# Optimization experiments

Hardware: AMD Instinct MI355X
Metric: run time of the kernel (lower is better)

## Reference

```python
import jax, jax.numpy as jnp
import numpy as np

DIM = 1024
HEADS = 16
DH = 64          # dim_for_head
INNER = HEADS * DH
SCALE = DH ** -0.5


def setup_inputs() -> dict:
    key = jax.random.key(0)
    ks = jax.random.split(key, 5)
    x = jax.random.normal(ks[0], (4, 2048, DIM), dtype=jnp.float32)
    ln_gamma = jnp.ones((DIM,), dtype=jnp.float32)
    ln_beta = jnp.zeros((DIM,), dtype=jnp.float32)
    # torch Linear weight is [out, in]; store same layout, apply as x @ W.T
    w_qkv = jax.random.normal(ks[1], (3 * INNER, DIM), dtype=jnp.float32) * (DIM ** -0.5)
    w_out = jax.random.normal(ks[2], (DIM, INNER), dtype=jnp.float32) * (INNER ** -0.5)
    b_out = jnp.zeros((DIM,), dtype=jnp.float32)
    return {"x": x, "ln_gamma": ln_gamma, "ln_beta": ln_beta,
            "w_qkv": w_qkv, "w_out": w_out, "b_out": b_out}


def reference(x, ln_gamma, ln_beta, w_qkv, w_out, b_out):
    b, n, d = x.shape
    # LayerNorm (eps=1e-5 as torch default)
    mu = jnp.mean(x, axis=-1, keepdims=True)
    var = jnp.mean(jnp.square(x - mu), axis=-1, keepdims=True)
    xn = (x - mu) * jax.lax.rsqrt(var + 1e-5) * ln_gamma + ln_beta
    # QKV projection
    qkv = xn @ w_qkv.T                                   # [b, n, 3*inner]
    q, k, v = jnp.split(qkv, 3, axis=-1)
    reshape = lambda t: t.reshape(b, n, HEADS, DH).transpose(0, 2, 1, 3)  # [b, h, n, d]
    q, k, v = reshape(q), reshape(k), reshape(v)
    # Attention
    dots = jnp.einsum('bhqd,bhkd->bhqk', q, k) * SCALE
    attn = jax.nn.softmax(dots, axis=-1)                 # dropout p=0 -> identity
    out = jnp.einsum('bhqk,bhkd->bhqd', attn, v)
    out = out.transpose(0, 2, 1, 3).reshape(b, n, INNER)
    return out @ w_out.T + b_out
```

## Files before the change

### kernel.cpp

```cpp
#include <hip/hip_runtime.h>
#include <stdint.h>


typedef __attribute__((ext_vector_type(4)))  float  f32x4;
typedef __attribute__((ext_vector_type(16))) float  f32x16;
typedef __attribute__((ext_vector_type(8)))  short  s16x8;
typedef __attribute__((ext_vector_type(4)))  unsigned short u16x4;
typedef __attribute__((ext_vector_type(2)))  int    i32x2;
typedef __attribute__((ext_vector_type(4)))  int    i32x4;

__device__ __forceinline__ float bf2f(short b) {
    union { unsigned u; float f; } x; x.u = ((unsigned)(unsigned short)b) << 16; return x.f;
}
__device__ __forceinline__ short f2bf(float f) {
    union { float f; unsigned u; } x; x.f = f;
    unsigned r = x.u + 0x7fffu + ((x.u >> 16) & 1u);
    return (short)(r >> 16);
}
__device__ __forceinline__ float exp2_hw(float x) {
    float r; asm("v_exp_f32 %0, %1" : "=v"(r) : "v"(x)); return r;
}

__device__ __forceinline__ void gload_lds16(const void* g, void* l) {
    __builtin_amdgcn_global_load_lds(
        (const __attribute__((address_space(1))) void*)g,
        (__attribute__((address_space(3))) void*)l, 16, 0, 0);
}

__global__ void cvt_bf16(const float* __restrict__ in, short* __restrict__ out, int n4) {
    int i = blockIdx.x * blockDim.x + threadIdx.x;
    if (i >= n4) return;
    f32x4 v = ((const f32x4*)in)[i];
    u16x4 o;
    o.x = (unsigned short)f2bf(v.x); o.y = (unsigned short)f2bf(v.y);
    o.z = (unsigned short)f2bf(v.z); o.w = (unsigned short)f2bf(v.w);
    ((u16x4*)out)[i] = o;
}

__global__ void cvt_wqkv(const float* __restrict__ in, short* __restrict__ out, int n4) {
    int i = blockIdx.x * blockDim.x + threadIdx.x;
    if (i >= n4) return;
    const int row = i >> 8;
    const float sc = (row < 1024) ? 0.18033688011112042f : 1.0f;
    f32x4 v = ((const f32x4*)in)[i];
    u16x4 o;
    o.x = (unsigned short)f2bf(v.x * sc); o.y = (unsigned short)f2bf(v.y * sc);
    o.z = (unsigned short)f2bf(v.z * sc); o.w = (unsigned short)f2bf(v.w * sc);
    ((u16x4*)out)[i] = o;
}

__global__ __launch_bounds__(256)
void ln_kernel(const float* __restrict__ x, const float* __restrict__ gamma,
               const float* __restrict__ beta, short* __restrict__ xn) {
    const int w = threadIdx.x >> 6, l = threadIdx.x & 63;
    const size_t row = (size_t)blockIdx.x * 4 + w;
    const float* xr = x + row * 1024;
    f32x4 v[4];
    float sum = 0.f, ss = 0.f;
#pragma unroll
    for (int i = 0; i < 4; i++) {
        v[i] = *(const f32x4*)(xr + (l + 64 * i) * 4);
#pragma unroll
        for (int e = 0; e < 4; e++) { sum += v[i][e]; ss += v[i][e] * v[i][e]; }
    }
#pragma unroll
    for (int d = 1; d < 64; d <<= 1) { sum += __shfl_xor(sum, d); ss += __shfl_xor(ss, d); }
    const float mu   = sum * (1.f / 1024.f);
    const float var  = ss * (1.f / 1024.f) - mu * mu;
    const float rstd = rsqrtf(var + 1e-5f);
#pragma unroll
    for (int i = 0; i < 4; i++) {
        f32x4 g  = *(const f32x4*)(gamma + (l + 64 * i) * 4);
        f32x4 bt = *(const f32x4*)(beta  + (l + 64 * i) * 4);
        u16x4 o;
#pragma unroll
        for (int e = 0; e < 4; e++)
            o[e] = (unsigned short)f2bf((v[i][e] - mu) * rstd * g[e] + bt[e]);
        *(u16x4*)(xn + row * 1024 + (l + 64 * i) * 4) = o;
    }
}

template <int NX>
__global__ __launch_bounds__(512, 2)
void gemm256(const short* __restrict__ A, const short* __restrict__ W,
             short* __restrict__ outb, int M, int N, int K) {
    extern __shared__ short smem[];
    short* Albuf = smem;
    short* Blbuf = smem + 32768;
    const int tid = threadIdx.x;
    const int w = tid >> 6, l = tid & 63;
    const int wr = w >> 2, wc = w & 3;
    const int nb = gridDim.x, bid = blockIdx.x;
    const int swz = (bid & 7) * (nb >> 3) + (bid >> 3);
    const int m0 = (swz / NX) * 256, n0 = (swz % NX) * 192;
    const int lx = l & 15, hi4 = l >> 4, l7 = l & 7;
    const int srow = l >> 3;
    const int scs  = (l & 7) ^ srow;

    f32x4 acc[8][3];
#pragma unroll
    for (int i = 0; i < 8; i++)
#pragma unroll
        for (int j = 0; j < 3; j++) acc[i][j] = (f32x4)0.f;

    auto STAGE = [&](int buf, int t) {
        const int k0 = t * 64;
#pragma unroll
        for (int p = 0; p < 4; p++) {
            const int row = p * 64 + w * 8 + srow;
            gload_lds16(A + (size_t)(m0 + row) * K + k0 + scs * 8,
                        Albuf + buf * 16384 + (p * 64 + w * 8) * 64);
        }
#pragma unroll
        for (int p = 0; p < 3; p++) {
            const int row = p * 64 + w * 8 + srow;
            gload_lds16(W + (size_t)(n0 + row) * K + k0 + scs * 8,
                        Blbuf + buf * 12288 + (p * 64 + w * 8) * 64);
        }
    };

    STAGE(0, 0);
    const int NT = K >> 6;
    for (int t = 0; t < NT; ++t) {
        const int cur = t & 1;
        if (t + 1 < NT) {
            STAGE(cur ^ 1, t + 1);
            asm volatile("s_waitcnt vmcnt(7)" ::: "memory");
        } else {
            asm volatile("s_waitcnt vmcnt(0)" ::: "memory");
        }
        __builtin_amdgcn_s_barrier();
        const short* Ab = Albuf + cur * 16384;
        const short* Bb = Blbuf + cur * 12288;

        s16x8 bfr[2][3];
#pragma unroll
        for (int kc = 0; kc < 2; kc++)
#pragma unroll
            for (int j = 0; j < 3; j++) {
                const int R = wc * 48 + j * 16 + lx;
                bfr[kc][j] = *(const s16x8*)(Bb + R * 64 + (((kc * 4 + hi4) ^ l7) * 8));
            }

#pragma unroll
        for (int p = 0; p < 4; p++) {
            s16x8 afr[2][2];
#pragma unroll
            for (int ii = 0; ii < 2; ii++)
#pragma unroll
                for (int kc = 0; kc < 2; kc++) {
                    const int R = wr * 128 + (p * 2 + ii) * 16 + lx;
                    afr[ii][kc] = *(const s16x8*)(Ab + R * 64 + (((kc * 4 + hi4) ^ l7) * 8));
                }
            __builtin_amdgcn_s_barrier();
            __builtin_amdgcn_s_setprio(1);
#pragma unroll
            for (int kc = 0; kc < 2; kc++)
#pragma unroll
                for (int ii = 0; ii < 2; ii++)
#pragma unroll
                    for (int j = 0; j < 3; j++)
                        acc[p * 2 + ii][j] = __builtin_amdgcn_mfma_f32_16x16x32_bf16(
                            afr[ii][kc], bfr[kc][j], acc[p * 2 + ii][j], 0, 0, 0);
            __builtin_amdgcn_s_setprio(0);
            __builtin_amdgcn_s_barrier();
        }
    }

    const int lr = hi4 * 4;
#pragma unroll
    for (int i = 0; i < 8; i++) {
        const int rb = m0 + wr * 128 + i * 16 + lr;
#pragma unroll
        for (int j = 0; j < 3; j++) {
            const int cc = n0 + wc * 48 + j * 16 + lx;
#pragma unroll
            for (int r = 0; r < 4; r++)
                outb[(size_t)(rb + r) * N + cc] = f2bf(acc[i][j][r]);
        }
    }
}

template <int MODE, int NX>
__global__ __launch_bounds__(256)
void gemm_bt(const short* __restrict__ A, const short* __restrict__ W,
             short* __restrict__ outb, float* __restrict__ outf,
             const float* __restrict__ bias, int M, int N, int K) {
    __shared__ short Al[128 * 64];
    __shared__ short Bl[128 * 64];
    const int tid = threadIdx.x;
    const int w = tid >> 6, l = tid & 63;
    const int wr = w >> 1, wc = w & 1;
    const int nb = gridDim.x, bid = blockIdx.x;
    const int swz = (bid & 7) * (nb >> 3) + (bid >> 3);
    const int m0 = (swz / NX) * 128, n0 = (swz % NX) * 128;
    const int r8 = tid >> 3;
    const int c8 = tid & 7;

    f32x4 acc[4][4];
#pragma unroll
    for (int i = 0; i < 4; i++)
#pragma unroll
        for (int j = 0; j < 4; j++) acc[i][j] = (f32x4)0.f;

    for (int k0 = 0; k0 < K; k0 += 64) {
        __syncthreads();
#pragma unroll
        for (int p = 0; p < 4; p++) {
            const int row = p * 32 + r8;
            gload_lds16(A + (size_t)(m0 + row) * K + k0 + c8 * 8, Al + (p * 32 + w * 8) * 64);
            gload_lds16(W + (size_t)(n0 + row) * K + k0 + c8 * 8, Bl + (p * 32 + w * 8) * 64);
        }
        __syncthreads();
#pragma unroll
        for (int kc = 0; kc < 2; kc++) {
            const int ko = kc * 32 + (l >> 4) * 8;
            s16x8 af[4], bf[4];
#pragma unroll
            for (int i = 0; i < 4; i++)
                af[i] = *(const s16x8*)(Al + (wr * 64 + i * 16 + (l & 15)) * 64 + ko);
#pragma unroll
            for (int j = 0; j < 4; j++)
                bf[j] = *(const s16x8*)(Bl + (wc * 64 + j * 16 + (l & 15)) * 64 + ko);
#pragma unroll
            for (int i = 0; i < 4; i++)
#pragma unroll
                for (int j = 0; j < 4; j++)
                    acc[i][j] = __builtin_amdgcn_mfma_f32_16x16x32_bf16(af[i], bf[j], acc[i][j], 0, 0, 0);
        }
    }

    const int lr = (l >> 4) * 4, lc = l & 15;
#pragma unroll
    for (int j = 0; j < 4; j++) {
        const int cc = n0 + wc * 64 + j * 16 + lc;
        const float bv = (MODE == 1) ? bias[cc] : 0.f;
#pragma unroll
        for (int i = 0; i < 4; i++) {
            const int rb = m0 + wr * 64 + i * 16 + lr;
#pragma unroll
            for (int r = 0; r < 4; r++) {
                const float vv = acc[i][j][r];
                if (MODE == 0) outb[(size_t)(rb + r) * N + cc] = f2bf(vv);
                else           outf[(size_t)(rb + r) * N + cc] = vv + bv;
            }
        }
    }
}

__global__ __launch_bounds__(256)
void transpose_v(const short* __restrict__ qkv, short* __restrict__ vt) {
    __shared__ short T[64 * 72];
    const int tid = threadIdx.x;
    const int bh = blockIdx.y;
    const int b = bh >> 4, h = bh & 15;
    const int k0 = blockIdx.x * 64;
    const short* Vp = qkv + (size_t)b * 2048 * 3072 + 2048 + h * 64;
    const int r = tid >> 3, c = tid & 7;
#pragma unroll
    for (int p = 0; p < 2; p++) {
        const int k = p * 32 + r;
        s16x8 v = *(const s16x8*)(Vp + (size_t)(k0 + k) * 3072 + c * 8);
        *(s16x8*)(&T[k * 72 + c * 8]) = v;
    }
    __syncthreads();
#pragma unroll
    for (int p = 0; p < 2; p++) {
        const int d = p * 32 + r;
        s16x8 o;
#pragma unroll
        for (int e = 0; e < 8; e++) o[e] = T[(c * 8 + e) * 72 + d];
        *(s16x8*)(vt + ((size_t)bh * 64 + d) * 2048 + k0 + c * 8) = o;
    }
}

__global__ __launch_bounds__(256, 2)
void attn_kernel(const short* __restrict__ qkv, const short* __restrict__ vtg,
                 short* __restrict__ aout) {
    __shared__ short KV[2][2][64 * 64];
    const int tid = threadIdx.x, w = tid >> 6, l = tid & 63;
    const int bid = blockIdx.x;
    const int swz = (bid & 7) * 64 + (bid >> 3);
    const int qt = swz & 7, bh = swz >> 3;
    const int b = bh >> 4, h = bh & 15;
    const int q0 = qt * 256;
    const int y = l & 31, hi = l >> 5, l7 = l & 7;
    const short* Qp  = qkv + (size_t)b * 2048 * 3072 + h * 64;
    const short* Kp  = Qp + 1024;
    const short* Vtp = vtg + (size_t)bh * 64 * 2048;

    s16x8 bq[2][4];
#pragma unroll
    for (int u = 0; u < 2; u++) {
        const int qrow = q0 + w * 64 + u * 32 + y;
#pragma unroll
        for (int kc = 0; kc < 4; kc++)
            bq[u][kc] = *(const s16x8*)(Qp + (size_t)qrow * 3072 + kc * 16 + hi * 8);
    }

    f32x16 oc[2][2], ls[2];
#pragma unroll
    for (int u = 0; u < 2; u++) { oc[u][0] = (f32x16)0.f; oc[u][1] = (f32x16)0.f; ls[u] = (f32x16)0.f; }

    s16x8 ones;
#pragma unroll
    for (int e = 0; e < 8; e++) ones[e] = (short)0x3F80;

    const int srow = l >> 3;
    const int scs  = (l & 7) ^ srow;
    auto stage = [&](int par, int kv) {
#pragma unroll
        for (int p = 0; p < 2; p++) {
            const int row = w * 16 + p * 8 + srow;
            gload_lds16(Kp  + (size_t)(kv + row) * 3072 + scs * 8, &KV[par][0][(w * 16 + p * 8) * 64]);
            gload_lds16(Vtp + (size_t)row * 2048 + kv + scs * 8,   &KV[par][1][(w * 16 + p * 8) * 64]);
        }
    };

    const int Abase = y * 64 + ((hi ^ (l7 & 1)) * 8);
    int cofs[4];
#pragma unroll
    for (int j = 0; j < 4; j++) cofs[j] = ((l7 >> 1) ^ j) * 16;

    auto tilestep = [&](int par, int kv) {
        __syncthreads();
        if (kv + 64 < 2048) stage(par ^ 1, kv + 64);
        const short* Kb = &KV[par][0][0];
        const short* Vb = &KV[par][1][0];

        f32x16 s[2][2];
        s[0][0] = (f32x16)0.f; s[0][1] = (f32x16)0.f;
        s[1][0] = (f32x16)0.f; s[1][1] = (f32x16)0.f;
        __builtin_amdgcn_s_setprio(1);
#pragma unroll
        for (int kc = 0; kc < 4; kc++) {
#pragma unroll
            for (int kb = 0; kb < 2; kb++) {
                s16x8 ak = *(const s16x8*)(Kb + kb * 2048 + Abase + cofs[kc]);
                s[0][kb] = __builtin_amdgcn_mfma_f32_32x32x16_bf16(ak, bq[0][kc], s[0][kb], 0, 0, 0);
                s[1][kb] = __builtin_amdgcn_mfma_f32_32x32x16_bf16(ak, bq[1][kc], s[1][kb], 0, 0, 0);
            }
        }
        __builtin_amdgcn_s_setprio(0);

        int W0[2][2][8];
#pragma unroll
        for (int u = 0; u < 2; u++) {
#pragma unroll
            for (int kb = 0; kb < 2; kb++)
#pragma unroll
                for (int r = 0; r < 16; r++) s[u][kb][r] = exp2_hw(s[u][kb][r]);
#pragma unroll
            for (int kb = 0; kb < 2; kb++)
#pragma unroll
                for (int i = 0; i < 8; i++)
                    asm("v_cvt_pk_bf16_f32 %0, %1, %2"
                        : "=v"(W0[u][kb][i]) : "v"(s[u][kb][2 * i]), "v"(s[u][kb][2 * i + 1]));
        }

        __builtin_amdgcn_s_setprio(1);
#pragma unroll
        for (int a = 0; a < 2; a++)
#pragma unroll
            for (int bb = 0; bb < 2; bb++) {
                const int st = a * 2 + bb;
                s16x8 bv0 = *(const s16x8*)(Vb + 0 * 2048 + Abase + cofs[st]);
                s16x8 bv1 = *(const s16x8*)(Vb + 1 * 2048 + Abase + cofs[st]);
#pragma unroll
                for (int u = 0; u < 2; u++) {
                    i32x2 r0 = __builtin_amdgcn_permlane32_swap(W0[u][a][4 * bb + 0], W0[u][a][4 * bb + 2], false, false);
                    i32x2 r1 = __builtin_amdgcn_permlane32_swap(W0[u][a][4 * bb + 1], W0[u][a][4 * bb + 3], false, false);
                    union { i32x4 wv; s16x8 hv; } uu;
                    uu.wv = (i32x4){r0.x, r1.x, r0.y, r1.y};
                    ls[u]    = __builtin_amdgcn_mfma_f32_32x32x16_bf16(uu.hv, ones, ls[u], 0, 0, 0);
                    oc[u][0] = __builtin_amdgcn_mfma_f32_32x32x16_bf16(uu.hv, bv0, oc[u][0], 0, 0, 0);
                    oc[u][1] = __builtin_amdgcn_mfma_f32_32x32x16_bf16(uu.hv, bv1, oc[u][1], 0, 0, 0);
                }
            }
        __builtin_amdgcn_s_setprio(0);
    };

    stage(0, 0);
    for (int kv = 0; kv < 2048; kv += 128) {
        tilestep(0, kv);
        tilestep(1, kv + 64);
    }

#pragma unroll
    for (int u = 0; u < 2; u++)
#pragma unroll
        for (int r = 0; r < 16; r++) {
            const int qrr = (r & 3) + 8 * (r >> 2) + 4 * hi;
            const float ivr = 1.f / ls[u][r];
            const size_t row = (size_t)b * 2048 + q0 + w * 64 + u * 32 + qrr;
#pragma unroll
            for (int t2 = 0; t2 < 2; t2++)
                aout[row * 1024 + h * 64 + t2 * 32 + y] = f2bf(oc[u][t2][r] * ivr);
        }
}

extern "C" void kernel_launch(void* const* d_in, const int* in_sizes, int n_in,
                              void* d_out, int out_size, void* d_ws, size_t ws_size,
                              hipStream_t stream) {
    const float* x    = (const float*)d_in[0];
    const float* g    = (const float*)d_in[1];
    const float* be   = (const float*)d_in[2];
    const float* wqkv = (const float*)d_in[3];
    const float* wout = (const float*)d_in[4];
    const float* bo   = (const float*)d_in[5];
    float* out = (float*)d_out;

    char* ws = (char*)d_ws;
    short* xn    = (short*)(ws);
    short* wqkvb = (short*)(ws + 16777216);
    short* woutb = (short*)(ws + 16777216 + 6291456);
    short* qkvb  = (short*)(ws + 25165824);
    short* attb  = (short*)(ws + 75497472);
    short* vtg   = xn;

    (void)hipFuncSetAttribute((const void*)gemm256<16>,
                              hipFuncAttributeMaxDynamicSharedMemorySize, 114688);

    cvt_wqkv<<<dim3(3072), 256, 0, stream>>>(wqkv, wqkvb, 3145728 / 4);
    cvt_bf16<<<dim3(1024), 256, 0, stream>>>(wout, woutb, 1048576 / 4);
    ln_kernel<<<dim3(2048), 256, 0, stream>>>(x, g, be, xn);
    gemm256<16><<<dim3(512), 512, 114688, stream>>>(xn, wqkvb, qkvb, 8192, 3072, 1024);
    transpose_v<<<dim3(32, 64), 256, 0, stream>>>(qkvb, vtg);
    attn_kernel<<<dim3(512), 256, 0, stream>>>(qkvb, vtg, attb);
    gemm_bt<1, 8><<<dim3(512), 256, 0, stream>>>(attb, woutb, nullptr, out, bo, 8192, 1024, 1024);
}
```

Before: 187.0 us.

## Reuse pipelined 256-row GEMM for output projection and merge weight conversions

The simple 128x128 single-buffered output-projection GEMM is replaced by the templated double-buffered 256x128 gemm256 kernel, which gains a bias/fp32 output mode and a variable N-tile width. The two weight-conversion kernels are fused into one launch. This is meant to improve data reuse and load/compute overlap in the out-projection and to cut one launch. The out-projection grid drops to 256 blocks of 512 threads, which may underfill the GPU's compute units.

```diff
diff --git a/kernel.cpp b/kernel.cpp
--- a/kernel.cpp
+++ b/kernel.cpp
@@ -27,21 +27,16 @@
         (__attribute__((address_space(3))) void*)l, 16, 0, 0);
 }
 
-__global__ void cvt_bf16(const float* __restrict__ in, short* __restrict__ out, int n4) {
+__global__ void cvt_weights(const float* __restrict__ wqkv, const float* __restrict__ wout,
+                            short* __restrict__ wqkvb, short* __restrict__ woutb) {
     int i = blockIdx.x * blockDim.x + threadIdx.x;
-    if (i >= n4) return;
-    f32x4 v = ((const f32x4*)in)[i];
-    u16x4 o;
-    o.x = (unsigned short)f2bf(v.x); o.y = (unsigned short)f2bf(v.y);
-    o.z = (unsigned short)f2bf(v.z); o.w = (unsigned short)f2bf(v.w);
-    ((u16x4*)out)[i] = o;
-}
-
-__global__ void cvt_wqkv(const float* __restrict__ in, short* __restrict__ out, int n4) {
-    int i = blockIdx.x * blockDim.x + threadIdx.x;
-    if (i >= n4) return;
-    const int row = i >> 8;
-    const float sc = (row < 1024) ? 0.18033688011112042f : 1.0f;
+    const float* in; short* out; float sc = 1.0f;
+    if (i < 786432) {
+        in = wqkv; out = wqkvb;
+        if ((i >> 8) < 1024) sc = 0.18033688011112042f;
+    } else {
+        i -= 786432; in = wout; out = woutb;
+    }
     f32x4 v = ((const f32x4*)in)[i];
     u16x4 o;
     o.x = (unsigned short)f2bf(v.x * sc); o.y = (unsigned short)f2bf(v.y * sc);
@@ -80,10 +75,11 @@
     }
 }
 
-template <int NX>
+template <int NX, int NJ, int MODE>
 __global__ __launch_bounds__(512, 2)
 void gemm256(const short* __restrict__ A, const short* __restrict__ W,
-             short* __restrict__ outb, int M, int N, int K) {
+             short* __restrict__ outb, float* __restrict__ outf,
+             const float* __restrict__ bias, int M, int N, int K) {
     extern __shared__ short smem[];
     short* Albuf = smem;
     short* Blbuf = smem + 32768;
@@ -92,16 +88,16 @@
     const int wr = w >> 2, wc = w & 3;
     const int nb = gridDim.x, bid = blockIdx.x;
     const int swz = (bid & 7) * (nb >> 3) + (bid >> 3);
-    const int m0 = (swz / NX) * 256, n0 = (swz % NX) * 192;
+    const int m0 = (swz / NX) * 256, n0 = (swz % NX) * (NJ * 64);
     const int lx = l & 15, hi4 = l >> 4, l7 = l & 7;
     const int srow = l >> 3;
     const int scs  = (l & 7) ^ srow;
 
-    f32x4 acc[8][3];
+    f32x4 acc[8][NJ];
 #pragma unroll
     for (int i = 0; i < 8; i++)
 #pragma unroll
-        for (int j = 0; j < 3; j++) acc[i][j] = (f32x4)0.f;
+        for (int j = 0; j < NJ; j++) acc[i][j] = (f32x4)0.f;
 
     auto STAGE = [&](int buf, int t) {
         const int k0 = t * 64;
@@ -112,10 +108,10 @@
                         Albuf + buf * 16384 + (p * 64 + w * 8) * 64);
         }
 #pragma unroll
-        for (int p = 0; p < 3; p++) {
+        for (int p = 0; p < NJ; p++) {
             const int row = p * 64 + w * 8 + srow;
             gload_lds16(W + (size_t)(n0 + row) * K + k0 + scs * 8,
-                        Blbuf + buf * 12288 + (p * 64 + w * 8) * 64);
+                        Blbuf + buf * (NJ * 4096) + (p * 64 + w * 8) * 64);
         }
     };
 
@@ -125,20 +121,21 @@
         const int cur = t & 1;
         if (t + 1 < NT) {
             STAGE(cur ^ 1, t + 1);
-            asm volatile("s_waitcnt vmcnt(7)" ::: "memory");
+            if constexpr (NJ == 3) asm volatile("s_waitcnt vmcnt(7)" ::: "memory");
+            else                   asm volatile("s_waitcnt vmcnt(6)" ::: "memory");
         } else {
             asm volatile("s_waitcnt vmcnt(0)" ::: "memory");
         }
         __builtin_amdgcn_s_barrier();
         const short* Ab = Albuf + cur * 16384;
-        const short* Bb = Blbuf + cur * 12288;
-
-        s16x8 bfr[2][3];
+        const short* Bb = Blbuf + cur * (NJ * 4096);
+
+        s16x8 bfr[2][NJ];
 #pragma unroll
         for (int kc = 0; kc < 2; kc++)
 #pragma unroll
-            for (int j = 0; j < 3; j++) {
-                const int R = wc * 48 + j * 16 + lx;
+            for (int j = 0; j < NJ; j++) {
+                const int R = wc * (NJ * 16) + j * 16 + lx;
                 bfr[kc][j] = *(const s16x8*)(Bb + R * 64 + (((kc * 4 + hi4) ^ l7) * 8));
             }
 
@@ -159,7 +156,7 @@
 #pragma unroll
                 for (int ii = 0; ii < 2; ii++)
 #pragma unroll
-                    for (int j = 0; j < 3; j++)
+                    for (int j = 0; j < NJ; j++)
                         acc[p * 2 + ii][j] = __builtin_amdgcn_mfma_f32_16x16x32_bf16(
                             afr[ii][kc], bfr[kc][j], acc[p * 2 + ii][j], 0, 0, 0);
             __builtin_amdgcn_s_setprio(0);
@@ -172,77 +169,13 @@
     for (int i = 0; i < 8; i++) {
         const int rb = m0 + wr * 128 + i * 16 + lr;
 #pragma unroll
-        for (int j = 0; j < 3; j++) {
-            const int cc = n0 + wc * 48 + j * 16 + lx;
-#pragma unroll
-            for (int r = 0; r < 4; r++)
-                outb[(size_t)(rb + r) * N + cc] = f2bf(acc[i][j][r]);
-        }
-    }
-}
-
-template <int MODE, int NX>
-__global__ __launch_bounds__(256)
-void gemm_bt(const short* __restrict__ A, const short* __restrict__ W,
-             short* __restrict__ outb, float* __restrict__ outf,
-             const float* __restrict__ bias, int M, int N, int K) {
-    __shared__ short Al[128 * 64];
-    __shared__ short Bl[128 * 64];
-    const int tid = threadIdx.x;
-    const int w = tid >> 6, l = tid & 63;
-    const int wr = w >> 1, wc = w & 1;
-    const int nb = gridDim.x, bid = blockIdx.x;
-    const int swz = (bid & 7) * (nb >> 3) + (bid >> 3);
-    const int m0 = (swz / NX) * 128, n0 = (swz % NX) * 128;
-    const int r8 = tid >> 3;
-    const int c8 = tid & 7;
-
-    f32x4 acc[4][4];
-#pragma unroll
-    for (int i = 0; i < 4; i++)
-#pragma unroll
-        for (int j = 0; j < 4; j++) acc[i][j] = (f32x4)0.f;
-
-    for (int k0 = 0; k0 < K; k0 += 64) {
-        __syncthreads();
-#pragma unroll
-        for (int p = 0; p < 4; p++) {
-            const int row = p * 32 + r8;
-            gload_lds16(A + (size_t)(m0 + row) * K + k0 + c8 * 8, Al + (p * 32 + w * 8) * 64);
-            gload_lds16(W + (size_t)(n0 + row) * K + k0 + c8 * 8, Bl + (p * 32 + w * 8) * 64);
-        }
-        __syncthreads();
-#pragma unroll
-        for (int kc = 0; kc < 2; kc++) {
-            const int ko = kc * 32 + (l >> 4) * 8;
-            s16x8 af[4], bf[4];
-#pragma unroll
-            for (int i = 0; i < 4; i++)
-                af[i] = *(const s16x8*)(Al + (wr * 64 + i * 16 + (l & 15)) * 64 + ko);
-#pragma unroll
-            for (int j = 0; j < 4; j++)
-                bf[j] = *(const s16x8*)(Bl + (wc * 64 + j * 16 + (l & 15)) * 64 + ko);
-#pragma unroll
-            for (int i = 0; i < 4; i++)
-#pragma unroll
-                for (int j = 0; j < 4; j++)
-                    acc[i][j] = __builtin_amdgcn_mfma_f32_16x16x32_bf16(af[i], bf[j], acc[i][j], 0, 0, 0);
-        }
-    }
-
-    const int lr = (l >> 4) * 4, lc = l & 15;
-#pragma unroll
-    for (int j = 0; j < 4; j++) {
-        const int cc = n0 + wc * 64 + j * 16 + lc;
-        const float bv = (MODE == 1) ? bias[cc] : 0.f;
-#pragma unroll
-        for (int i = 0; i < 4; i++) {
-            const int rb = m0 + wr * 64 + i * 16 + lr;
+        for (int j = 0; j < NJ; j++) {
+            const int cc = n0 + wc * (NJ * 16) + j * 16 + lx;
+            const float bv = (MODE == 1) ? bias[cc] : 0.f;
 #pragma unroll
             for (int r = 0; r < 4; r++) {
-                const float vv = acc[i][j][r];
-                if (MODE == 0) outb[(size_t)(rb + r) * N + cc] = f2bf(vv);
-                else           outf[(size_t)(rb + r) * N + cc] = vv + bv;
+                if (MODE == 0) outb[(size_t)(rb + r) * N + cc] = f2bf(acc[i][j][r]);
+                else           outf[(size_t)(rb + r) * N + cc] = acc[i][j][r] + bv;
             }
         }
     }
@@ -418,14 +351,15 @@
     short* attb  = (short*)(ws + 75497472);
     short* vtg   = xn;
 
-    (void)hipFuncSetAttribute((const void*)gemm256<16>,
+    (void)hipFuncSetAttribute((const void*)gemm256<16, 3, 0>,
                               hipFuncAttributeMaxDynamicSharedMemorySize, 114688);
-
-    cvt_wqkv<<<dim3(3072), 256, 0, stream>>>(wqkv, wqkvb, 3145728 / 4);
-    cvt_bf16<<<dim3(1024), 256, 0, stream>>>(wout, woutb, 1048576 / 4);
+    (void)hipFuncSetAttribute((const void*)gemm256<8, 2, 1>,
+                              hipFuncAttributeMaxDynamicSharedMemorySize, 98304);
+
+    cvt_weights<<<dim3(4096), 256, 0, stream>>>(wqkv, wout, wqkvb, woutb);
     ln_kernel<<<dim3(2048), 256, 0, stream>>>(x, g, be, xn);
-    gemm256<16><<<dim3(512), 512, 114688, stream>>>(xn, wqkvb, qkvb, 8192, 3072, 1024);
+    gemm256<16, 3, 0><<<dim3(512), 512, 114688, stream>>>(xn, wqkvb, qkvb, nullptr, nullptr, 8192, 3072, 1024);
     transpose_v<<<dim3(32, 64), 256, 0, stream>>>(qkvb, vtg);
     attn_kernel<<<dim3(512), 256, 0, stream>>>(qkvb, vtg, attb);
-    gemm_bt<1, 8><<<dim3(512), 256, 0, stream>>>(attb, woutb, nullptr, out, bo, 8192, 1024, 1024);
-}
+    gemm256<8, 2, 1><<<dim3(256), 512, 98304, stream>>>(attb, woutb, nullptr, out, bo, 8192, 1024, 1024);
+}
```

Result: faster. 179.3 us (-4.1%).
